# Kernel tuning notes

Hardware: AMD Instinct MI355X
Metric: run time of the kernel (lower is better)

Reference implementation:

```python
import jax, jax.numpy as jnp
import numpy as np

N_NODES = 50000
N_EDGES = 400000
N_GRAPHS = 32
EMB = 64
EDGE_DIM = 4
IN_DIM = 11
LAYERS = 4
EPS = 1e-5


def _bn(x, g, b):
    # BatchNorm1d in train mode: biased batch statistics over rows
    m = jnp.mean(x, axis=0)
    v = jnp.mean(jnp.square(x - m), axis=0)
    return g * (x - m) * jax.lax.rsqrt(v + EPS) + b


def setup_inputs() -> dict:
    key = jax.random.key(0)
    ks = jax.random.split(key, 16)
    x = jax.random.normal(ks[0], (N_NODES, IN_DIM), dtype=jnp.float32)
    edge_attr = jax.random.normal(ks[1], (N_EDGES, EDGE_DIM), dtype=jnp.float32)
    edge_index = jax.random.randint(ks[2], (2, N_EDGES), 0, N_NODES, dtype=jnp.int32)
    batch = jnp.sort(jax.random.randint(ks[3], (N_NODES,), 0, N_GRAPHS, dtype=jnp.int32))

    def lin(k, fan_in, shape):
        bound = 1.0 / np.sqrt(fan_in)
        return jax.random.uniform(k, shape, jnp.float32, -bound, bound)

    msg_in = 2 * EMB + EDGE_DIM  # 132
    upd_in = 2 * EMB             # 128
    kk = jax.random.split(ks[4], 12)
    params = dict(
        lin_in_W=lin(kk[0], IN_DIM, (IN_DIM, EMB)),
        lin_in_b=lin(kk[1], IN_DIM, (EMB,)),
        msg_W1=lin(kk[2], msg_in, (LAYERS, msg_in, EMB)),
        msg_b1=lin(kk[3], msg_in, (LAYERS, EMB)),
        msg_g1=jnp.ones((LAYERS, EMB), jnp.float32),
        msg_be1=jnp.zeros((LAYERS, EMB), jnp.float32),
        msg_W2=lin(kk[4], EMB, (LAYERS, EMB, EMB)),
        msg_b2=lin(kk[5], EMB, (LAYERS, EMB)),
        msg_g2=jnp.ones((LAYERS, EMB), jnp.float32),
        msg_be2=jnp.zeros((LAYERS, EMB), jnp.float32),
        upd_W1=lin(kk[6], upd_in, (LAYERS, upd_in, EMB)),
        upd_b1=lin(kk[7], upd_in, (LAYERS, EMB)),
        upd_g1=jnp.ones((LAYERS, EMB), jnp.float32),
        upd_be1=jnp.zeros((LAYERS, EMB), jnp.float32),
        upd_W2=lin(kk[8], EMB, (LAYERS, EMB, EMB)),
        upd_b2=lin(kk[9], EMB, (LAYERS, EMB)),
        upd_g2=jnp.ones((LAYERS, EMB), jnp.float32),
        upd_be2=jnp.zeros((LAYERS, EMB), jnp.float32),
        pred_W=lin(kk[10], EMB, (EMB, 1)),
        pred_b=lin(kk[11], EMB, (1,)),
    )
    return dict(x=x, edge_attr=edge_attr, edge_index=edge_index, batch=batch, **params)


def reference(x, edge_attr, edge_index, batch, lin_in_W, lin_in_b,
              msg_W1, msg_b1, msg_g1, msg_be1, msg_W2, msg_b2, msg_g2, msg_be2,
              upd_W1, upd_b1, upd_g1, upd_be1, upd_W2, upd_b2, upd_g2, upd_be2,
              pred_W, pred_b):
    src = edge_index[0]  # j (source)
    dst = edge_index[1]  # i (target, PyG default flow source_to_target)
    h = x @ lin_in_W + lin_in_b  # (n, d)
    for l in range(LAYERS):
        m_in = jnp.concatenate([h[dst], h[src], edge_attr], axis=-1)  # (e, 2d+d_e)
        m = jax.nn.relu(_bn(m_in @ msg_W1[l] + msg_b1[l], msg_g1[l], msg_be1[l]))
        m = jax.nn.relu(_bn(m @ msg_W2[l] + msg_b2[l], msg_g2[l], msg_be2[l]))
        aggr = jax.ops.segment_sum(m, dst, num_segments=N_NODES)  # scatter-add
        u_in = jnp.concatenate([h, aggr], axis=-1)  # (n, 2d)
        u = jax.nn.relu(_bn(u_in @ upd_W1[l] + upd_b1[l], upd_g1[l], upd_be1[l]))
        u = jax.nn.relu(_bn(u @ upd_W2[l] + upd_b2[l], upd_g2[l], upd_be2[l]))
        h = h + u  # residual in MPNNModel.forward
    sums = jax.ops.segment_sum(h, batch, num_segments=N_GRAPHS)
    counts = jax.ops.segment_sum(jnp.ones((h.shape[0],), h.dtype), batch, num_segments=N_GRAPHS)
    h_graph = sums / jnp.maximum(counts, 1.0)[:, None]  # global_mean_pool
    out = h_graph @ pred_W + pred_b  # (G, 1)
    return out.reshape(-1)
```

## Files before the change

kernel.cpp:

```cpp
#include <hip/hip_runtime.h>

#define DEV __device__ __forceinline__

constexpr int NN = 50000;
constexpr int NE = 400000;
constexpr int NG = 32;
constexpr float EPSV = 1e-5f;
constexpr int SCAN_BLOCKS = 196;
constexpr int NSHARD = 8;
constexpr int STB = NSHARD * 128;

typedef __attribute__((ext_vector_type(8))) short s16x8;
typedef __attribute__((ext_vector_type(4))) float f32x4;

DEV unsigned short f2b(float f) {
  union { float f; unsigned u; } x; x.f = f;
  unsigned r = x.u + 0x7fffu + ((x.u >> 16) & 1u);
  return (unsigned short)(r >> 16);
}
DEV float b2f(unsigned short u) {
  union { unsigned u; float f; } x; x.u = ((unsigned)u) << 16; return x.f;
}

DEV s16x8 frag_from_f32(const float* p) {
  const float4 v0 = *(const float4*)p;
  const float4 v1 = *(const float4*)(p + 4);
  s16x8 af;
  af[0] = (short)f2b(v0.x); af[1] = (short)f2b(v0.y);
  af[2] = (short)f2b(v0.z); af[3] = (short)f2b(v0.w);
  af[4] = (short)f2b(v1.x); af[5] = (short)f2b(v1.y);
  af[6] = (short)f2b(v1.z); af[7] = (short)f2b(v1.w);
  return af;
}

DEV void bn_coeff(const float* __restrict__ st, const float* __restrict__ g,
                  const float* __restrict__ be, float invM, int c,
                  float& sc, float& sh) {
  float s = 0.f, s2 = 0.f;
#pragma unroll
  for (int k = 0; k < NSHARD; ++k) {
    s += st[k * 128 + c];
    s2 += st[k * 128 + 64 + c];
  }
  float mean = s * invM;
  float var = s2 * invM - mean * mean;
  sc = g[c] * rsqrtf(var + EPSV);
  sh = be[c] - mean * sc;
}

__global__ __launch_bounds__(256) void lin_in_kernel(
    const float* __restrict__ x, const float* __restrict__ W,
    const float* __restrict__ b, float* __restrict__ h)
{
  int gid = blockIdx.x * 256 + threadIdx.x;
  if (gid >= NN * 64) return;
  int n = gid >> 6, c = gid & 63;
  float acc = b[c];
#pragma unroll
  for (int k = 0; k < 11; ++k)
    acc = fmaf(x[n * 11 + k], W[k * 64 + c], acc);
  h[gid] = acc;
}

__global__ __launch_bounds__(256) void hist_kernel(
    const int* __restrict__ dstI, int* __restrict__ deg)
{
  int e = blockIdx.x * 256 + threadIdx.x;
  if (e < NE) atomicAdd(&deg[dstI[e]], 1);
}

__global__ __launch_bounds__(256) void scan_pass1(
    const int* __restrict__ deg, int* __restrict__ blockSums)
{
  __shared__ int red[4];
  int tid = threadIdx.x;
  int idx = blockIdx.x * 256 + tid;
  int v = (idx < NN) ? deg[idx] : 0;
#pragma unroll
  for (int off = 32; off > 0; off >>= 1) v += __shfl_down(v, off, 64);
  if ((tid & 63) == 0) red[tid >> 6] = v;
  __syncthreads();
  if (tid == 0) blockSums[blockIdx.x] = red[0] + red[1] + red[2] + red[3];
}

__global__ __launch_bounds__(256) void scan_pass2(
    const int* __restrict__ blockSums, int* __restrict__ blockOffs)
{
  __shared__ int part[256];
  int tid = threadIdx.x;
  int v = (tid < SCAN_BLOCKS) ? blockSums[tid] : 0;
  part[tid] = v;
  __syncthreads();
  for (int off = 1; off < 256; off <<= 1) {
    int t = 0;
    if (tid >= off) t = part[tid - off];
    __syncthreads();
    if (tid >= off) part[tid] += t;
    __syncthreads();
  }
  blockOffs[tid] = (tid == 0) ? 0 : part[tid - 1];
}

__global__ __launch_bounds__(256) void scan_pass3(
    const int* __restrict__ deg, const int* __restrict__ blockOffs,
    int* __restrict__ rowptr, int* __restrict__ cursor)
{
  __shared__ int part[256];
  int tid = threadIdx.x;
  int idx = blockIdx.x * 256 + tid;
  int v = (idx < NN) ? deg[idx] : 0;
  part[tid] = v;
  __syncthreads();
  for (int off = 1; off < 256; off <<= 1) {
    int t = 0;
    if (tid >= off) t = part[tid - off];
    __syncthreads();
    if (tid >= off) part[tid] += t;
    __syncthreads();
  }
  int excl = (tid == 0) ? 0 : part[tid - 1];
  int val = blockOffs[blockIdx.x] + excl;
  if (idx < NN) { rowptr[idx] = val; cursor[idx] = val; }
  if (idx == 0) rowptr[NN] = NE;
}

__global__ __launch_bounds__(256) void fill_permute_kernel(
    const int* __restrict__ srcI, const int* __restrict__ dstI,
    const float* __restrict__ ea, int* __restrict__ cursor,
    int* __restrict__ srcP, int* __restrict__ dstP,
    float* __restrict__ eaP)
{
  int e = blockIdx.x * 256 + threadIdx.x;
  if (e < NE) {
    int d = dstI[e];
    int pos = atomicAdd(&cursor[d], 1);
    srcP[pos] = srcI[e];
    dstP[pos] = d;
    *(float4*)&eaP[(size_t)pos * 4] = *(const float4*)&ea[(size_t)e * 4];
  }
}

__global__ __launch_bounds__(256) void gemm_dual_mfma(
    const float* __restrict__ h, const float* __restrict__ W,
    unsigned short* __restrict__ Hd, unsigned short* __restrict__ Hs)
{
  __shared__ __align__(16) unsigned short Wt_s[2 * 64 * 72];

  const int tid = threadIdx.x;
  const int lane = tid & 63;
  const int wave = tid >> 6;
  const int nn = lane & 15;
  const int kq = lane >> 4;

#pragma unroll
  for (int i = 0; i < 32; ++i) {
    int idx = i * 256 + tid;
    int half = idx >> 12;
    int rem = idx & 4095;
    int k = rem >> 6, n = rem & 63;
    Wt_s[half * 4608 + n * 72 + k] = f2b(W[idx]);
  }
  __syncthreads();

  s16x8 bfrag[2][4][2];
#pragma unroll
  for (int o = 0; o < 2; ++o)
#pragma unroll
    for (int nt = 0; nt < 4; ++nt)
#pragma unroll
      for (int kc = 0; kc < 2; ++kc) {
        const unsigned short* p =
            &Wt_s[o * 4608 + (nt * 16 + nn) * 72 + kc * 32 + kq * 8];
#pragma unroll
        for (int j = 0; j < 8; ++j) bfrag[o][nt][kc][j] = (short)p[j];
      }

  const int rbase = blockIdx.x * 128 + wave * 32;

  f32x4 acc[2][2][4];
#pragma unroll
  for (int o = 0; o < 2; ++o)
#pragma unroll
    for (int rt = 0; rt < 2; ++rt)
#pragma unroll
      for (int nt = 0; nt < 4; ++nt) acc[o][rt][nt] = (f32x4){0.f, 0.f, 0.f, 0.f};

#pragma unroll
  for (int rt = 0; rt < 2; ++rt) {
    int row = rbase + rt * 16 + nn;
    int rowc = row < NN ? row : NN - 1;
#pragma unroll
    for (int kc = 0; kc < 2; ++kc) {
      s16x8 af = frag_from_f32(&h[(size_t)rowc * 64 + kc * 32 + kq * 8]);
#pragma unroll
      for (int o = 0; o < 2; ++o)
#pragma unroll
        for (int nt = 0; nt < 4; ++nt)
          acc[o][rt][nt] = __builtin_amdgcn_mfma_f32_16x16x32_bf16(
              af, bfrag[o][nt][kc], acc[o][rt][nt], 0, 0, 0);
    }
  }

#pragma unroll
  for (int rt = 0; rt < 2; ++rt)
#pragma unroll
    for (int nt = 0; nt < 4; ++nt) {
      int col = nt * 16 + nn;
#pragma unroll
      for (int reg = 0; reg < 4; ++reg) {
        int row = rbase + rt * 16 + kq * 4 + reg;
        if (row < NN) {
          Hd[(size_t)row * 64 + col] = f2b(acc[0][rt][nt][reg]);
          Hs[(size_t)row * 64 + col] = f2b(acc[1][rt][nt][reg]);
        }
      }
    }
}

__global__ __launch_bounds__(256) void edge_combine(
    const unsigned short* __restrict__ Hd, const unsigned short* __restrict__ Hs,
    const float* __restrict__ eaP, const int* __restrict__ srcP,
    const int* __restrict__ dstP, const float* __restrict__ Wb,
    const float* __restrict__ bias, unsigned short* __restrict__ t1,
    float* __restrict__ outStats)
{
  __shared__ float red_s[128];
  const int tid = threadIdx.x;
  const int c0 = (tid & 7) * 8;
  float bv[8], w0[8], w1[8], w2[8], w3[8];
#pragma unroll
  for (int j = 0; j < 8; ++j) {
    bv[j] = bias[c0 + j];
    w0[j] = Wb[0 * 64 + c0 + j];
    w1[j] = Wb[1 * 64 + c0 + j];
    w2[j] = Wb[2 * 64 + c0 + j];
    w3[j] = Wb[3 * 64 + c0 + j];
  }

  float s[8], s2[8];
#pragma unroll
  for (int j = 0; j < 8; ++j) { s[j] = 0.f; s2[j] = 0.f; }

  const int e0 = (blockIdx.x * 256 + tid) >> 3;
  const int estep = (gridDim.x * 256) >> 3;

  for (int e = e0; e < NE; e += 2 * estep) {
    int eb = e + estep;
    bool hasB = eb < NE;
    int siA = srcP[e], diA = dstP[e];
    float4 avA = *(const float4*)&eaP[(size_t)e * 4];
    uint4 hdA = *(const uint4*)&Hd[(size_t)diA * 64 + c0];
    uint4 hsA = *(const uint4*)&Hs[(size_t)siA * 64 + c0];
    int ebc = hasB ? eb : e;
    int siB = srcP[ebc], diB = dstP[ebc];
    float4 avB = *(const float4*)&eaP[(size_t)ebc * 4];
    uint4 hdB = *(const uint4*)&Hd[(size_t)diB * 64 + c0];
    uint4 hsB = *(const uint4*)&Hs[(size_t)siB * 64 + c0];

    {
      const unsigned hdw[4] = {hdA.x, hdA.y, hdA.z, hdA.w};
      const unsigned hsw[4] = {hsA.x, hsA.y, hsA.z, hsA.w};
      unsigned short ob[8];
#pragma unroll
      for (int d = 0; d < 4; ++d) {
        union { unsigned u; float f; } a0, a1, b0, b1;
        a0.u = (hdw[d] & 0xffffu) << 16; a1.u = hdw[d] & 0xffff0000u;
        b0.u = (hsw[d] & 0xffffu) << 16; b1.u = hsw[d] & 0xffff0000u;
        int j0 = d * 2, j1 = d * 2 + 1;
        float y0 = a0.f + b0.f + bv[j0] + avA.x * w0[j0] + avA.y * w1[j0] + avA.z * w2[j0] + avA.w * w3[j0];
        float y1 = a1.f + b1.f + bv[j1] + avA.x * w0[j1] + avA.y * w1[j1] + avA.z * w2[j1] + avA.w * w3[j1];
        ob[j0] = f2b(y0); ob[j1] = f2b(y1);
        s[j0] += y0; s2[j0] += y0 * y0;
        s[j1] += y1; s2[j1] += y1 * y1;
      }
      *(uint4*)&t1[(size_t)e * 64 + c0] = *(const uint4*)ob;
    }
    if (hasB) {
      const unsigned hdw[4] = {hdB.x, hdB.y, hdB.z, hdB.w};
      const unsigned hsw[4] = {hsB.x, hsB.y, hsB.z, hsB.w};
      unsigned short ob[8];
#pragma unroll
      for (int d = 0; d < 4; ++d) {
        union { unsigned u; float f; } a0, a1, b0, b1;
        a0.u = (hdw[d] & 0xffffu) << 16; a1.u = hdw[d] & 0xffff0000u;
        b0.u = (hsw[d] & 0xffffu) << 16; b1.u = hsw[d] & 0xffff0000u;
        int j0 = d * 2, j1 = d * 2 + 1;
        float y0 = a0.f + b0.f + bv[j0] + avB.x * w0[j0] + avB.y * w1[j0] + avB.z * w2[j0] + avB.w * w3[j0];
        float y1 = a1.f + b1.f + bv[j1] + avB.x * w0[j1] + avB.y * w1[j1] + avB.z * w2[j1] + avB.w * w3[j1];
        ob[j0] = f2b(y0); ob[j1] = f2b(y1);
        s[j0] += y0; s2[j0] += y0 * y0;
        s[j1] += y1; s2[j1] += y1 * y1;
      }
      *(uint4*)&t1[(size_t)eb * 64 + c0] = *(const uint4*)ob;
    }
  }
#pragma unroll
  for (int j = 0; j < 8; ++j) {
    s[j] += __shfl_xor(s[j], 8, 64);
    s[j] += __shfl_xor(s[j], 16, 64);
    s[j] += __shfl_xor(s[j], 32, 64);
    s2[j] += __shfl_xor(s2[j], 8, 64);
    s2[j] += __shfl_xor(s2[j], 16, 64);
    s2[j] += __shfl_xor(s2[j], 32, 64);
  }
  if (tid < 128) red_s[tid] = 0.f;
  __syncthreads();
  if ((tid & 63) < 8) {
#pragma unroll
    for (int j = 0; j < 8; ++j) {
      atomicAdd(&red_s[c0 + j], s[j]);
      atomicAdd(&red_s[64 + c0 + j], s2[j]);
    }
  }
  __syncthreads();
  if (tid < 128)
    atomicAdd(&outStats[(blockIdx.x & (NSHARD - 1)) * 128 + tid], red_s[tid]);
}

__global__ __launch_bounds__(256) void gemm64_bn_mfma(
    const unsigned short* A0,
    const float* __restrict__ W,
    const float* __restrict__ bias,
    const float* __restrict__ inStats,
    const float* __restrict__ inG,
    const float* __restrict__ inBe,
    float invM_in,
    unsigned short* outp,
    float* __restrict__ outStats,
    int M)
{
  __shared__ __align__(16) unsigned short Wt_s[64 * 72];
  __shared__ float scale_s[64];
  __shared__ float shift_s[64];
  __shared__ float red_s[128];

  const int tid = threadIdx.x;
  const int lane = tid & 63;
  const int wave = tid >> 6;
  const int nn = lane & 15;
  const int kq = lane >> 4;

  if (tid < 64) {
    float sc, sh;
    bn_coeff(inStats, inG, inBe, invM_in, tid, sc, sh);
    scale_s[tid] = sc;
    shift_s[tid] = sh;
  }
#pragma unroll
  for (int i = 0; i < 16; ++i) {
    int idx = i * 256 + tid;
    int k = idx >> 6, n = idx & 63;
    Wt_s[n * 72 + k] = f2b(W[idx]);
  }
  __syncthreads();

  s16x8 bfrag[4][2];
#pragma unroll
  for (int nt = 0; nt < 4; ++nt)
#pragma unroll
    for (int kc = 0; kc < 2; ++kc)
      bfrag[nt][kc] = *(const s16x8*)&Wt_s[(nt * 16 + nn) * 72 + kc * 32 + kq * 8];

  float scf[2][8], shf[2][8];
#pragma unroll
  for (int kc = 0; kc < 2; ++kc) {
    int k0 = kc * 32 + kq * 8;
    float4 a = *(const float4*)&scale_s[k0];
    float4 b = *(const float4*)&scale_s[k0 + 4];
    float4 c = *(const float4*)&shift_s[k0];
    float4 d = *(const float4*)&shift_s[k0 + 4];
    scf[kc][0] = a.x; scf[kc][1] = a.y; scf[kc][2] = a.z; scf[kc][3] = a.w;
    scf[kc][4] = b.x; scf[kc][5] = b.y; scf[kc][6] = b.z; scf[kc][7] = b.w;
    shf[kc][0] = c.x; shf[kc][1] = c.y; shf[kc][2] = c.z; shf[kc][3] = c.w;
    shf[kc][4] = d.x; shf[kc][5] = d.y; shf[kc][6] = d.z; shf[kc][7] = d.w;
  }

  const int rbase = blockIdx.x * 256 + wave * 64;

  f32x4 acc[4][4];
#pragma unroll
  for (int rt = 0; rt < 4; ++rt)
#pragma unroll
    for (int nt = 0; nt < 4; ++nt) acc[rt][nt] = (f32x4){0.f, 0.f, 0.f, 0.f};

  uint4 raw[4][2];
#pragma unroll
  for (int rt = 0; rt < 4; ++rt) {
    int row = rbase + rt * 16 + nn;
    int rowc = row < M ? row : M - 1;
#pragma unroll
    for (int kc = 0; kc < 2; ++kc)
      raw[rt][kc] = *(const uint4*)&A0[(size_t)rowc * 64 + kc * 32 + kq * 8];
  }

#pragma unroll
  for (int rt = 0; rt < 4; ++rt) {
#pragma unroll
    for (int kc = 0; kc < 2; ++kc) {
      unsigned wbits[4] = {raw[rt][kc].x, raw[rt][kc].y, raw[rt][kc].z, raw[rt][kc].w};
      s16x8 af;
#pragma unroll
      for (int d = 0; d < 4; ++d) {
        union { unsigned u; float f; } lo, hi;
        lo.u = (wbits[d] & 0xffffu) << 16;
        hi.u = wbits[d] & 0xffff0000u;
        int j0 = d * 2, j1 = d * 2 + 1;
        af[j0] = (short)f2b(fmaxf(fmaf(scf[kc][j0], lo.f, shf[kc][j0]), 0.f));
        af[j1] = (short)f2b(fmaxf(fmaf(scf[kc][j1], hi.f, shf[kc][j1]), 0.f));
      }
#pragma unroll
      for (int nt = 0; nt < 4; ++nt)
        acc[rt][nt] = __builtin_amdgcn_mfma_f32_16x16x32_bf16(
            af, bfrag[nt][kc], acc[rt][nt], 0, 0, 0);
    }
  }

  float bcol[4];
#pragma unroll
  for (int nt = 0; nt < 4; ++nt) bcol[nt] = bias[nt * 16 + nn];

  float s[4] = {0.f, 0.f, 0.f, 0.f};
  float s2[4] = {0.f, 0.f, 0.f, 0.f};
#pragma unroll
  for (int rt = 0; rt < 4; ++rt)
#pragma unroll
    for (int nt = 0; nt < 4; ++nt) {
      int col = nt * 16 + nn;
#pragma unroll
      for (int reg = 0; reg < 4; ++reg) {
        int row = rbase + rt * 16 + kq * 4 + reg;
        if (row < M) {
          float y = acc[rt][nt][reg] + bcol[nt];
          outp[(size_t)row * 64 + col] = f2b(y);
          s[nt] += y; s2[nt] += y * y;
        }
      }
    }
#pragma unroll
  for (int nt = 0; nt < 4; ++nt) {
    s[nt] += __shfl_xor(s[nt], 16, 64);
    s[nt] += __shfl_xor(s[nt], 32, 64);
    s2[nt] += __shfl_xor(s2[nt], 16, 64);
    s2[nt] += __shfl_xor(s2[nt], 32, 64);
  }
  if (tid < 128) red_s[tid] = 0.f;
  __syncthreads();
  if (lane < 16) {
#pragma unroll
    for (int nt = 0; nt < 4; ++nt) {
      atomicAdd(&red_s[nt * 16 + nn], s[nt]);
      atomicAdd(&red_s[64 + nt * 16 + nn], s2[nt]);
    }
  }
  __syncthreads();
  if (tid < 128)
    atomicAdd(&outStats[(blockIdx.x & (NSHARD - 1)) * 128 + tid], red_s[tid]);
}

__global__ __launch_bounds__(256) void gemm_concat_mfma(
    const float* __restrict__ A0,
    const unsigned short* __restrict__ A1b,
    const float* __restrict__ W,
    const float* __restrict__ bias,
    unsigned short* __restrict__ outp,
    float* __restrict__ outStats,
    int M)
{
  __shared__ __align__(16) unsigned short Wt_s[64 * 136];
  __shared__ float red_s[128];

  const int tid = threadIdx.x;
  const int lane = tid & 63;
  const int wave = tid >> 6;
  const int nn = lane & 15;
  const int kq = lane >> 4;

#pragma unroll
  for (int i = 0; i < 32; ++i) {
    int idx = i * 256 + tid;
    int k = idx >> 6, n = idx & 63;
    Wt_s[n * 136 + k] = f2b(W[idx]);
  }
  __syncthreads();

  s16x8 bfrag[4][4];
#pragma unroll
  for (int nt = 0; nt < 4; ++nt)
#pragma unroll
    for (int kc = 0; kc < 4; ++kc) {
      const unsigned short* p = &Wt_s[(nt * 16 + nn) * 136 + kc * 32 + kq * 8];
#pragma unroll
      for (int j = 0; j < 8; ++j) bfrag[nt][kc][j] = (short)p[j];
    }

  const int rbase = blockIdx.x * 128 + wave * 32;

  f32x4 acc[2][4];
#pragma unroll
  for (int rt = 0; rt < 2; ++rt)
#pragma unroll
    for (int nt = 0; nt < 4; ++nt) acc[rt][nt] = (f32x4){0.f, 0.f, 0.f, 0.f};

#pragma unroll
  for (int rt = 0; rt < 2; ++rt) {
    int row = rbase + rt * 16 + nn;
    int rowc = row < M ? row : M - 1;
#pragma unroll
    for (int kc = 0; kc < 4; ++kc) {
      s16x8 af;
      if (kc < 2) {
        af = frag_from_f32(&A0[(size_t)rowc * 64 + kc * 32 + kq * 8]);
      } else {
        af = *(const s16x8*)&A1b[(size_t)rowc * 64 + (kc - 2) * 32 + kq * 8];
      }
#pragma unroll
      for (int nt = 0; nt < 4; ++nt)
        acc[rt][nt] = __builtin_amdgcn_mfma_f32_16x16x32_bf16(
            af, bfrag[nt][kc], acc[rt][nt], 0, 0, 0);
    }
  }

  float bcol[4];
#pragma unroll
  for (int nt = 0; nt < 4; ++nt) bcol[nt] = bias[nt * 16 + nn];

  float s[4] = {0.f, 0.f, 0.f, 0.f};
  float s2[4] = {0.f, 0.f, 0.f, 0.f};
#pragma unroll
  for (int rt = 0; rt < 2; ++rt)
#pragma unroll
    for (int nt = 0; nt < 4; ++nt) {
      int col = nt * 16 + nn;
#pragma unroll
      for (int reg = 0; reg < 4; ++reg) {
        int row = rbase + rt * 16 + kq * 4 + reg;
        if (row < M) {
          float y = acc[rt][nt][reg] + bcol[nt];
          outp[(size_t)row * 64 + col] = f2b(y);
          s[nt] += y; s2[nt] += y * y;
        }
      }
    }
#pragma unroll
  for (int nt = 0; nt < 4; ++nt) {
    s[nt] += __shfl_xor(s[nt], 16, 64);
    s[nt] += __shfl_xor(s[nt], 32, 64);
    s2[nt] += __shfl_xor(s2[nt], 16, 64);
    s2[nt] += __shfl_xor(s2[nt], 32, 64);
  }
  if (tid < 128) red_s[tid] = 0.f;
  __syncthreads();
  if (lane < 16) {
#pragma unroll
    for (int nt = 0; nt < 4; ++nt) {
      atomicAdd(&red_s[nt * 16 + nn], s[nt]);
      atomicAdd(&red_s[64 + nt * 16 + nn], s2[nt]);
    }
  }
  __syncthreads();
  if (tid < 128)
    atomicAdd(&outStats[(blockIdx.x & (NSHARD - 1)) * 128 + tid], red_s[tid]);
}

__global__ __launch_bounds__(256) void aggregate_kernel(
    const unsigned short* __restrict__ t2, const int* __restrict__ rowptr,
    const float* __restrict__ stats, const float* __restrict__ g,
    const float* __restrict__ be, float invM,
    unsigned short* __restrict__ aggr)
{
  __shared__ float sc_s[64], sh_s[64];
  const int tid = threadIdx.x;
  if (tid < 64) {
    float sc, sh;
    bn_coeff(stats, g, be, invM, tid, sc, sh);
    sc_s[tid] = sc;
    sh_s[tid] = sh;
  }
  __syncthreads();

  int node = (blockIdx.x * 256 + tid) >> 6;
  int lane = tid & 63;
  if (node >= NN) return;
  const int c8 = (lane & 7) * 8;
  const int rq = lane >> 3;

  float sc[8], sh[8];
#pragma unroll
  for (int j = 0; j < 8; ++j) {
    sc[j] = sc_s[c8 + j];
    sh[j] = sh_s[c8 + j];
  }

  int lo = rowptr[node], hi = rowptr[node + 1];
  float acc[8] = {0.f, 0.f, 0.f, 0.f, 0.f, 0.f, 0.f, 0.f};

  for (int i = lo; i < hi; i += 16) {
    int r0 = i + rq;
    int r1 = i + 8 + rq;
    bool h0 = r0 < hi, h1 = r1 < hi;
    uint4 v0 = make_uint4(0u, 0u, 0u, 0u), v1 = make_uint4(0u, 0u, 0u, 0u);
    if (h0) v0 = *(const uint4*)&t2[(size_t)r0 * 64 + c8];
    if (h1) v1 = *(const uint4*)&t2[(size_t)r1 * 64 + c8];
    if (h0) {
      const unsigned w[4] = {v0.x, v0.y, v0.z, v0.w};
#pragma unroll
      for (int d = 0; d < 4; ++d) {
        union { unsigned u; float f; } a0, a1;
        a0.u = (w[d] & 0xffffu) << 16;
        a1.u = w[d] & 0xffff0000u;
        acc[d * 2] += fmaxf(fmaf(sc[d * 2], a0.f, sh[d * 2]), 0.f);
        acc[d * 2 + 1] += fmaxf(fmaf(sc[d * 2 + 1], a1.f, sh[d * 2 + 1]), 0.f);
      }
    }
    if (h1) {
      const unsigned w[4] = {v1.x, v1.y, v1.z, v1.w};
#pragma unroll
      for (int d = 0; d < 4; ++d) {
        union { unsigned u; float f; } a0, a1;
        a0.u = (w[d] & 0xffffu) << 16;
        a1.u = w[d] & 0xffff0000u;
        acc[d * 2] += fmaxf(fmaf(sc[d * 2], a0.f, sh[d * 2]), 0.f);
        acc[d * 2 + 1] += fmaxf(fmaf(sc[d * 2 + 1], a1.f, sh[d * 2 + 1]), 0.f);
      }
    }
  }
#pragma unroll
  for (int j = 0; j < 8; ++j) {
    acc[j] += __shfl_xor(acc[j], 8, 64);
    acc[j] += __shfl_xor(acc[j], 16, 64);
    acc[j] += __shfl_xor(acc[j], 32, 64);
  }
  if (rq == 0) {
    unsigned short o[8];
#pragma unroll
    for (int j = 0; j < 8; ++j) o[j] = f2b(acc[j]);
    *(uint4*)&aggr[(size_t)node * 64 + c8] = *(const uint4*)o;
  }
}

__global__ __launch_bounds__(256) void residual_kernel(
    const unsigned short* __restrict__ u2, const float* __restrict__ stats,
    const float* __restrict__ g, const float* __restrict__ be,
    float invM, float* __restrict__ h)
{
  __shared__ float sc_s[64], sh_s[64];
  const int tid = threadIdx.x;
  if (tid < 64) {
    float sc, sh;
    bn_coeff(stats, g, be, invM, tid, sc, sh);
    sc_s[tid] = sc;
    sh_s[tid] = sh;
  }
  __syncthreads();

  int gid = blockIdx.x * 256 + tid;
  if (gid >= NN * 16) return;
  int c = (gid & 15) * 4;
  ushort4 v4 = *(const ushort4*)&u2[(size_t)gid * 4];
  float4 hv = *(const float4*)&h[(size_t)gid * 4];
  const unsigned short vu[4] = {v4.x, v4.y, v4.z, v4.w};
  float* hp = (float*)&hv;
#pragma unroll
  for (int j = 0; j < 4; ++j)
    hp[j] += fmaxf(fmaf(sc_s[c + j], b2f(vu[j]), sh_s[c + j]), 0.f);
  *(float4*)&h[(size_t)gid * 4] = hv;
}

constexpr int POOL_NPB = 128;

__global__ __launch_bounds__(256) void pool_partial(
    const float* __restrict__ h, const int* __restrict__ batch,
    float* __restrict__ sums)
{
  int lane = threadIdx.x & 63;
  int wave = threadIdx.x >> 6;
  int base = blockIdx.x * POOL_NPB;
  float acc = 0.f;
  int gcur = -1;
  for (int i = wave; i < POOL_NPB; i += 4) {
    int n = base + i;
    if (n >= NN) break;
    int g = batch[n];
    if (g != gcur) {
      if (gcur >= 0) atomicAdd(&sums[gcur * 64 + lane], acc);
      gcur = g;
      acc = 0.f;
    }
    acc += h[(size_t)n * 64 + lane];
  }
  if (gcur >= 0) atomicAdd(&sums[gcur * 64 + lane], acc);
}

DEV int lower_bound_i(const int* __restrict__ a, int n, int v) {
  int lo = 0, hi = n;
  while (lo < hi) {
    int m = (lo + hi) >> 1;
    if (a[m] < v) lo = m + 1; else hi = m;
  }
  return lo;
}

__global__ __launch_bounds__(64) void pool_final(
    const float* __restrict__ sums, const int* __restrict__ batch,
    const float* __restrict__ predW, const float* __restrict__ predB,
    float* __restrict__ out)
{
  int g = blockIdx.x;
  int lane = threadIdx.x;
  int lo = lower_bound_i(batch, NN, g);
  int hi = lower_bound_i(batch, NN, g + 1);
  float cnt = fmaxf((float)(hi - lo), 1.0f);
  float p = sums[g * 64 + lane] / cnt * predW[lane];
#pragma unroll
  for (int off = 32; off > 0; off >>= 1) p += __shfl_down(p, off, 64);
  if (lane == 0) out[g] = p + predB[0];
}

extern "C" void kernel_launch(void* const* d_in, const int* in_sizes, int n_in,
                              void* d_out, int out_size, void* d_ws, size_t ws_size,
                              hipStream_t stream)
{
  (void)in_sizes; (void)n_in; (void)out_size; (void)ws_size;

  const float* x        = (const float*)d_in[0];
  const float* edge_attr= (const float*)d_in[1];
  const int*   eidx     = (const int*)d_in[2];
  const int*   batch    = (const int*)d_in[3];
  const float* linW     = (const float*)d_in[4];
  const float* linB     = (const float*)d_in[5];
  const float* msgW1    = (const float*)d_in[6];
  const float* msgB1    = (const float*)d_in[7];
  const float* msgG1    = (const float*)d_in[8];
  const float* msgBe1   = (const float*)d_in[9];
  const float* msgW2    = (const float*)d_in[10];
  const float* msgB2    = (const float*)d_in[11];
  const float* msgG2    = (const float*)d_in[12];
  const float* msgBe2   = (const float*)d_in[13];
  const float* updW1    = (const float*)d_in[14];
  const float* updB1    = (const float*)d_in[15];
  const float* updG1    = (const float*)d_in[16];
  const float* updBe1   = (const float*)d_in[17];
  const float* updW2    = (const float*)d_in[18];
  const float* updB2    = (const float*)d_in[19];
  const float* updG2    = (const float*)d_in[20];
  const float* updBe2   = (const float*)d_in[21];
  const float* predW    = (const float*)d_in[22];
  const float* predB    = (const float*)d_in[23];

  const int* srcI = eidx;
  const int* dstI = eidx + NE;

  char* p = (char*)d_ws;
  float* h  = (float*)p;            p += (size_t)NN * 64 * 4;
  unsigned short* t1 = (unsigned short*)p; p += (size_t)NE * 64 * 2;
  unsigned short* aggr = (unsigned short*)p; p += (size_t)NN * 64 * 2;
  unsigned short* u1 = (unsigned short*)p;   p += (size_t)NN * 64 * 2;
  unsigned short* Hd = (unsigned short*)p;   p += (size_t)NN * 64 * 2;
  unsigned short* Hs = (unsigned short*)p;   p += (size_t)NN * 64 * 2;
  float* stats = (float*)p;         p += 16 * STB * 4;
  float* sums = (float*)p;          p += NG * 64 * 4;
  int* deg = (int*)p;               p += (size_t)NN * 4;
  int* cursor = (int*)p;            p += (size_t)NN * 4;
  int* rowptr = (int*)p;            p += (size_t)(NN + 1) * 4;
  int* srcP = (int*)p;              p += (size_t)NE * 4;
  int* dstP = (int*)p;              p += (size_t)NE * 4;
  float* eaP = (float*)p;           p += (size_t)NE * 4 * 4;
  int* blockSums = (int*)p;         p += 256 * 4;
  int* blockOffs = (int*)p;         p += 256 * 4;

  hipMemsetAsync(stats, 0, (16 * STB + NG * 64) * sizeof(float), stream);
  hipMemsetAsync(deg, 0, NN * sizeof(int), stream);

  hist_kernel<<<(NE + 255) / 256, 256, 0, stream>>>(dstI, deg);
  scan_pass1<<<SCAN_BLOCKS, 256, 0, stream>>>(deg, blockSums);
  scan_pass2<<<1, 256, 0, stream>>>(blockSums, blockOffs);
  scan_pass3<<<SCAN_BLOCKS, 256, 0, stream>>>(deg, blockOffs, rowptr, cursor);
  fill_permute_kernel<<<(NE + 255) / 256, 256, 0, stream>>>(
      srcI, dstI, edge_attr, cursor, srcP, dstP, eaP);

  lin_in_kernel<<<(NN * 64 + 255) / 256, 256, 0, stream>>>(x, linW, linB, h);

  const float invE = 1.0f / (float)NE;
  const float invN = 1.0f / (float)NN;
  const int NB128 = (NN + 127) / 128;
  const int NB256 = (NN + 255) / 256;
  const int EB256 = (NE + 255) / 256;

  for (int l = 0; l < 4; ++l) {
    float* st0 = stats + (l * 4 + 0) * STB;
    float* st1 = stats + (l * 4 + 1) * STB;
    float* st2 = stats + (l * 4 + 2) * STB;
    float* st3 = stats + (l * 4 + 3) * STB;
    const float* W1 = msgW1 + (size_t)l * 132 * 64;

    gemm_dual_mfma<<<NB128, 256, 0, stream>>>(h, W1, Hd, Hs);

    edge_combine<<<2048, 256, 0, stream>>>(
        Hd, Hs, eaP, srcP, dstP, W1 + 128 * 64, msgB1 + l * 64,
        t1, st0);

    gemm64_bn_mfma<<<EB256, 256, 0, stream>>>(
        t1, msgW2 + (size_t)l * 64 * 64, msgB2 + l * 64,
        st0, msgG1 + l * 64, msgBe1 + l * 64, invE,
        t1, st1, NE);

    aggregate_kernel<<<(NN * 64 + 255) / 256, 256, 0, stream>>>(
        t1, rowptr, st1, msgG2 + l * 64, msgBe2 + l * 64, invE, aggr);

    gemm_concat_mfma<<<NB128, 256, 0, stream>>>(
        h, aggr, updW1 + (size_t)l * 128 * 64, updB1 + l * 64,
        u1, st2, NN);

    gemm64_bn_mfma<<<NB256, 256, 0, stream>>>(
        u1, updW2 + (size_t)l * 64 * 64, updB2 + l * 64,
        st2, updG1 + l * 64, updBe1 + l * 64, invN,
        u1, st3, NN);

    residual_kernel<<<(NN * 16 + 255) / 256, 256, 0, stream>>>(
        u1, st3, updG2 + l * 64, updBe2 + l * 64, invN, h);
  }

  pool_partial<<<(NN + POOL_NPB - 1) / POOL_NPB, 256, 0, stream>>>(h, batch, sums);
  pool_final<<<NG, 64, 0, stream>>>(sums, batch, predW, predB, (float*)d_out);
}
```

Before: 683.3 us.

## Split edge permutation, unroll edge_combine by four, process two row tiles per GEMM block

Edge sorting is split into two kernels. One records each edge's sorted position, and a second gathers src, dst and attributes in sorted order, so the writes become coalesced. The edge_combine loop now issues gathers for four edges before doing any compute, which exposes more memory-level parallelism. gemm64_bn_mfma now handles 512 rows per block and prefetches the second tile's rows while the first tile's output is written, which halves the grid and reuses the weight fragments and BN setup. The costs are an extra kernel launch and pass over eid, plus higher register pressure from the larger unrolls.

```diff
diff --git a/kernel.cpp b/kernel.cpp
--- a/kernel.cpp
+++ b/kernel.cpp
@@ -124,19 +124,29 @@
   if (idx == 0) rowptr[NN] = NE;
 }
 
-__global__ __launch_bounds__(256) void fill_permute_kernel(
-    const int* __restrict__ srcI, const int* __restrict__ dstI,
-    const float* __restrict__ ea, int* __restrict__ cursor,
+__global__ __launch_bounds__(256) void fill_pos_kernel(
+    const int* __restrict__ dstI, int* __restrict__ cursor,
+    int* __restrict__ eid)
+{
+  int e = blockIdx.x * 256 + threadIdx.x;
+  if (e < NE) {
+    int pos = atomicAdd(&cursor[dstI[e]], 1);
+    eid[pos] = e;
+  }
+}
+
+__global__ __launch_bounds__(256) void permute_kernel(
+    const int* __restrict__ eid, const int* __restrict__ srcI,
+    const int* __restrict__ dstI, const float* __restrict__ ea,
     int* __restrict__ srcP, int* __restrict__ dstP,
     float* __restrict__ eaP)
 {
-  int e = blockIdx.x * 256 + threadIdx.x;
-  if (e < NE) {
-    int d = dstI[e];
-    int pos = atomicAdd(&cursor[d], 1);
-    srcP[pos] = srcI[e];
-    dstP[pos] = d;
-    *(float4*)&eaP[(size_t)pos * 4] = *(const float4*)&ea[(size_t)e * 4];
+  int p = blockIdx.x * 256 + threadIdx.x;
+  if (p < NE) {
+    int e = eid[p];
+    srcP[p] = srcI[e];
+    dstP[p] = dstI[e];
+    *(float4*)&eaP[(size_t)p * 4] = *(const float4*)&ea[(size_t)e * 4];
   }
 }
 
@@ -244,54 +254,41 @@
   const int e0 = (blockIdx.x * 256 + tid) >> 3;
   const int estep = (gridDim.x * 256) >> 3;
 
-  for (int e = e0; e < NE; e += 2 * estep) {
-    int eb = e + estep;
-    bool hasB = eb < NE;
-    int siA = srcP[e], diA = dstP[e];
-    float4 avA = *(const float4*)&eaP[(size_t)e * 4];
-    uint4 hdA = *(const uint4*)&Hd[(size_t)diA * 64 + c0];
-    uint4 hsA = *(const uint4*)&Hs[(size_t)siA * 64 + c0];
-    int ebc = hasB ? eb : e;
-    int siB = srcP[ebc], diB = dstP[ebc];
-    float4 avB = *(const float4*)&eaP[(size_t)ebc * 4];
-    uint4 hdB = *(const uint4*)&Hd[(size_t)diB * 64 + c0];
-    uint4 hsB = *(const uint4*)&Hs[(size_t)siB * 64 + c0];
-
-    {
-      const unsigned hdw[4] = {hdA.x, hdA.y, hdA.z, hdA.w};
-      const unsigned hsw[4] = {hsA.x, hsA.y, hsA.z, hsA.w};
+  for (int e = e0; e < NE; e += 4 * estep) {
+    bool has[4];
+    uint4 hd[4], hs[4];
+    float4 av[4];
+    int eidx4[4];
+#pragma unroll
+    for (int u = 0; u < 4; ++u) {
+      int ee = e + u * estep;
+      has[u] = ee < NE;
+      int ec = has[u] ? ee : e;
+      eidx4[u] = ec;
+      int si = srcP[ec], di = dstP[ec];
+      av[u] = *(const float4*)&eaP[(size_t)ec * 4];
+      hd[u] = *(const uint4*)&Hd[(size_t)di * 64 + c0];
+      hs[u] = *(const uint4*)&Hs[(size_t)si * 64 + c0];
+    }
+#pragma unroll
+    for (int u = 0; u < 4; ++u) {
+      if (!has[u]) continue;
+      const unsigned hdw[4] = {hd[u].x, hd[u].y, hd[u].z, hd[u].w};
+      const unsigned hsw[4] = {hs[u].x, hs[u].y, hs[u].z, hs[u].w};
       unsigned short ob[8];
 #pragma unroll
       for (int d = 0; d < 4; ++d) {
-        union { unsigned u; float f; } a0, a1, b0, b1;
-        a0.u = (hdw[d] & 0xffffu) << 16; a1.u = hdw[d] & 0xffff0000u;
-        b0.u = (hsw[d] & 0xffffu) << 16; b1.u = hsw[d] & 0xffff0000u;
+        union { unsigned uu; float f; } a0, a1, b0, b1u;
+        a0.uu = (hdw[d] & 0xffffu) << 16; a1.uu = hdw[d] & 0xffff0000u;
+        b0.uu = (hsw[d] & 0xffffu) << 16; b1u.uu = hsw[d] & 0xffff0000u;
         int j0 = d * 2, j1 = d * 2 + 1;
-        float y0 = a0.f + b0.f + bv[j0] + avA.x * w0[j0] + avA.y * w1[j0] + avA.z * w2[j0] + avA.w * w3[j0];
-        float y1 = a1.f + b1.f + bv[j1] + avA.x * w0[j1] + avA.y * w1[j1] + avA.z * w2[j1] + avA.w * w3[j1];
+        float y0 = a0.f + b0.f + bv[j0] + av[u].x * w0[j0] + av[u].y * w1[j0] + av[u].z * w2[j0] + av[u].w * w3[j0];
+        float y1 = a1.f + b1u.f + bv[j1] + av[u].x * w0[j1] + av[u].y * w1[j1] + av[u].z * w2[j1] + av[u].w * w3[j1];
         ob[j0] = f2b(y0); ob[j1] = f2b(y1);
         s[j0] += y0; s2[j0] += y0 * y0;
         s[j1] += y1; s2[j1] += y1 * y1;
       }
-      *(uint4*)&t1[(size_t)e * 64 + c0] = *(const uint4*)ob;
-    }
-    if (hasB) {
-      const unsigned hdw[4] = {hdB.x, hdB.y, hdB.z, hdB.w};
-      const unsigned hsw[4] = {hsB.x, hsB.y, hsB.z, hsB.w};
-      unsigned short ob[8];
-#pragma unroll
-      for (int d = 0; d < 4; ++d) {
-        union { unsigned u; float f; } a0, a1, b0, b1;
-        a0.u = (hdw[d] & 0xffffu) << 16; a1.u = hdw[d] & 0xffff0000u;
-        b0.u = (hsw[d] & 0xffffu) << 16; b1.u = hsw[d] & 0xffff0000u;
-        int j0 = d * 2, j1 = d * 2 + 1;
-        float y0 = a0.f + b0.f + bv[j0] + avB.x * w0[j0] + avB.y * w1[j0] + avB.z * w2[j0] + avB.w * w3[j0];
-        float y1 = a1.f + b1.f + bv[j1] + avB.x * w0[j1] + avB.y * w1[j1] + avB.z * w2[j1] + avB.w * w3[j1];
-        ob[j0] = f2b(y0); ob[j1] = f2b(y1);
-        s[j0] += y0; s2[j0] += y0 * y0;
-        s[j1] += y1; s2[j1] += y1 * y1;
-      }
-      *(uint4*)&t1[(size_t)eb * 64 + c0] = *(const uint4*)ob;
+      *(uint4*)&t1[(size_t)eidx4[u] * 64 + c0] = *(const uint4*)ob;
     }
   }
 #pragma unroll
@@ -375,24 +372,30 @@
     shf[kc][4] = d.x; shf[kc][5] = d.y; shf[kc][6] = d.z; shf[kc][7] = d.w;
   }
 
-  const int rbase = blockIdx.x * 256 + wave * 64;
-
+  float bcol[4];
+#pragma unroll
+  for (int nt = 0; nt < 4; ++nt) bcol[nt] = bias[nt * 16 + nn];
+
+  float s[4] = {0.f, 0.f, 0.f, 0.f};
+  float s2[4] = {0.f, 0.f, 0.f, 0.f};
+
+  uint4 raw[4][2];
   f32x4 acc[4][4];
-#pragma unroll
-  for (int rt = 0; rt < 4; ++rt)
-#pragma unroll
-    for (int nt = 0; nt < 4; ++nt) acc[rt][nt] = (f32x4){0.f, 0.f, 0.f, 0.f};
-
-  uint4 raw[4][2];
+
+  const int rb0 = blockIdx.x * 512 + wave * 64;
 #pragma unroll
   for (int rt = 0; rt < 4; ++rt) {
-    int row = rbase + rt * 16 + nn;
+    int row = rb0 + rt * 16 + nn;
     int rowc = row < M ? row : M - 1;
 #pragma unroll
     for (int kc = 0; kc < 2; ++kc)
       raw[rt][kc] = *(const uint4*)&A0[(size_t)rowc * 64 + kc * 32 + kq * 8];
   }
 
+#pragma unroll
+  for (int rt = 0; rt < 4; ++rt)
+#pragma unroll
+    for (int nt = 0; nt < 4; ++nt) acc[rt][nt] = (f32x4){0.f, 0.f, 0.f, 0.f};
 #pragma unroll
   for (int rt = 0; rt < 4; ++rt) {
 #pragma unroll
@@ -415,12 +418,16 @@
     }
   }
 
-  float bcol[4];
-#pragma unroll
-  for (int nt = 0; nt < 4; ++nt) bcol[nt] = bias[nt * 16 + nn];
-
-  float s[4] = {0.f, 0.f, 0.f, 0.f};
-  float s2[4] = {0.f, 0.f, 0.f, 0.f};
+  const int rb1 = rb0 + 256;
+#pragma unroll
+  for (int rt = 0; rt < 4; ++rt) {
+    int row = rb1 + rt * 16 + nn;
+    int rowc = row < M ? row : M - 1;
+#pragma unroll
+    for (int kc = 0; kc < 2; ++kc)
+      raw[rt][kc] = *(const uint4*)&A0[(size_t)rowc * 64 + kc * 32 + kq * 8];
+  }
+
 #pragma unroll
   for (int rt = 0; rt < 4; ++rt)
 #pragma unroll
@@ -428,7 +435,7 @@
       int col = nt * 16 + nn;
 #pragma unroll
       for (int reg = 0; reg < 4; ++reg) {
-        int row = rbase + rt * 16 + kq * 4 + reg;
+        int row = rb0 + rt * 16 + kq * 4 + reg;
         if (row < M) {
           float y = acc[rt][nt][reg] + bcol[nt];
           outp[(size_t)row * 64 + col] = f2b(y);
@@ -436,6 +443,49 @@
         }
       }
     }
+
+#pragma unroll
+  for (int rt = 0; rt < 4; ++rt)
+#pragma unroll
+    for (int nt = 0; nt < 4; ++nt) acc[rt][nt] = (f32x4){0.f, 0.f, 0.f, 0.f};
+#pragma unroll
+  for (int rt = 0; rt < 4; ++rt) {
+#pragma unroll
+    for (int kc = 0; kc < 2; ++kc) {
+      unsigned wbits[4] = {raw[rt][kc].x, raw[rt][kc].y, raw[rt][kc].z, raw[rt][kc].w};
+      s16x8 af;
+#pragma unroll
+      for (int d = 0; d < 4; ++d) {
+        union { unsigned u; float f; } lo, hi;
+        lo.u = (wbits[d] & 0xffffu) << 16;
+        hi.u = wbits[d] & 0xffff0000u;
+        int j0 = d * 2, j1 = d * 2 + 1;
+        af[j0] = (short)f2b(fmaxf(fmaf(scf[kc][j0], lo.f, shf[kc][j0]), 0.f));
+        af[j1] = (short)f2b(fmaxf(fmaf(scf[kc][j1], hi.f, shf[kc][j1]), 0.f));
+      }
+#pragma unroll
+      for (int nt = 0; nt < 4; ++nt)
+        acc[rt][nt] = __builtin_amdgcn_mfma_f32_16x16x32_bf16(
+            af, bfrag[nt][kc], acc[rt][nt], 0, 0, 0);
+    }
+  }
+
+#pragma unroll
+  for (int rt = 0; rt < 4; ++rt)
+#pragma unroll
+    for (int nt = 0; nt < 4; ++nt) {
+      int col = nt * 16 + nn;
+#pragma unroll
+      for (int reg = 0; reg < 4; ++reg) {
+        int row = rb1 + rt * 16 + kq * 4 + reg;
+        if (row < M) {
+          float y = acc[rt][nt][reg] + bcol[nt];
+          outp[(size_t)row * 64 + col] = f2b(y);
+          s[nt] += y; s2[nt] += y * y;
+        }
+      }
+    }
+
 #pragma unroll
   for (int nt = 0; nt < 4; ++nt) {
     s[nt] += __shfl_xor(s[nt], 16, 64);
@@ -762,6 +812,7 @@
   int* deg = (int*)p;               p += (size_t)NN * 4;
   int* cursor = (int*)p;            p += (size_t)NN * 4;
   int* rowptr = (int*)p;            p += (size_t)(NN + 1) * 4;
+  int* eid = (int*)p;               p += (size_t)NE * 4;
   int* srcP = (int*)p;              p += (size_t)NE * 4;
   int* dstP = (int*)p;              p += (size_t)NE * 4;
   float* eaP = (float*)p;           p += (size_t)NE * 4 * 4;
@@ -775,16 +826,17 @@
   scan_pass1<<<SCAN_BLOCKS, 256, 0, stream>>>(deg, blockSums);
   scan_pass2<<<1, 256, 0, stream>>>(blockSums, blockOffs);
   scan_pass3<<<SCAN_BLOCKS, 256, 0, stream>>>(deg, blockOffs, rowptr, cursor);
-  fill_permute_kernel<<<(NE + 255) / 256, 256, 0, stream>>>(
-      srcI, dstI, edge_attr, cursor, srcP, dstP, eaP);
+  fill_pos_kernel<<<(NE + 255) / 256, 256, 0, stream>>>(dstI, cursor, eid);
+  permute_kernel<<<(NE + 255) / 256, 256, 0, stream>>>(
+      eid, srcI, dstI, edge_attr, srcP, dstP, eaP);
 
   lin_in_kernel<<<(NN * 64 + 255) / 256, 256, 0, stream>>>(x, linW, linB, h);
 
   const float invE = 1.0f / (float)NE;
   const float invN = 1.0f / (float)NN;
   const int NB128 = (NN + 127) / 128;
-  const int NB256 = (NN + 255) / 256;
-  const int EB256 = (NE + 255) / 256;
+  const int NB512 = (NN + 511) / 512;
+  const int EB512 = (NE + 511) / 512;
 
   for (int l = 0; l < 4; ++l) {
     float* st0 = stats + (l * 4 + 0) * STB;
@@ -799,7 +851,7 @@
         Hd, Hs, eaP, srcP, dstP, W1 + 128 * 64, msgB1 + l * 64,
         t1, st0);
 
-    gemm64_bn_mfma<<<EB256, 256, 0, stream>>>(
+    gemm64_bn_mfma<<<EB512, 256, 0, stream>>>(
         t1, msgW2 + (size_t)l * 64 * 64, msgB2 + l * 64,
         st0, msgG1 + l * 64, msgBe1 + l * 64, invE,
         t1, st1, NE);
@@ -811,7 +863,7 @@
         h, aggr, updW1 + (size_t)l * 128 * 64, updB1 + l * 64,
         u1, st2, NN);
 
-    gemm64_bn_mfma<<<NB256, 256, 0, stream>>>(
+    gemm64_bn_mfma<<<NB512, 256, 0, stream>>>(
         u1, updW2 + (size_t)l * 64 * 64, updB2 + l * 64,
         st2, updG1 + l * 64, updBe1 + l * 64, invN,
         u1, st3, NN);
```

Result: faster. 661.3 us (-3.2%).
